# Optimization experiments

Measured on AMD Instinct MI355X. Metric: run time of the kernel, lower is better.

Reference implementation:

```python
import jax, jax.numpy as jnp
import numpy as np

T, B, H = 256, 512, 2048

def setup_inputs() -> dict:
    key = jax.random.key(0)
    ks = jax.random.split(key, 10)
    s = 1.0 / np.sqrt(H)  # torch RNN/Linear init scale (values only need to be sane)
    return {
        "initial_input": jax.random.normal(ks[0], (B, 1), jnp.float32),
        "hidden": jax.random.normal(ks[1], (B, H), jnp.float32),
        "targets": jax.random.normal(ks[2], (T, B, 1), jnp.float32),
        "W_ih": jax.random.normal(ks[3], (H, 1), jnp.float32) * s,
        "b_ih": jax.random.normal(ks[4], (H,), jnp.float32) * s,
        "W_hh": jax.random.normal(ks[5], (H, H), jnp.float32) * s,
        "b_hh": jax.random.normal(ks[6], (H,), jnp.float32) * s,
        "W_out": jax.random.normal(ks[7], (1, H), jnp.float32) * s,
        "b_out": jax.random.normal(ks[8], (1,), jnp.float32) * s,
        "tf_mask": jax.random.randint(ks[9], (T,), 0, 2) > 0,  # per-step teacher-force decision
    }

def reference(initial_input, hidden, targets, W_ih, b_ih, W_hh, b_hh, W_out, b_out, tf_mask):
    def step(carry, xs):
        h, x = carry                      # h: [B,H], x: [B,1]
        tgt, tf = xs                      # tgt: [B,1], tf: scalar bool
        h = jnp.tanh(x @ W_ih.T + b_ih + h @ W_hh.T + b_hh)  # [B,H]
        y = h @ W_out.T + b_out           # [B,1]
        x_next = jnp.where(tf, tgt, y)
        return (h, x_next), y
    (_, _), outputs = jax.lax.scan(step, (hidden, initial_input), (targets, tf_mask))
    return outputs  # [T,B,1]
```

## Files before the change

### kernel.cpp

```cpp
#include <hip/hip_runtime.h>

using half8   = __attribute__((ext_vector_type(8))) _Float16;
using f32x16  = __attribute__((ext_vector_type(16))) float;
using float4v = __attribute__((ext_vector_type(4))) float;

#define T_STEPS 256
#define BATCH   512
#define HID     2048
#define KS      128

__device__ __forceinline__ f32x16 zero16() {
  f32x16 z;
#pragma unroll
  for (int r = 0; r < 16; ++r) z[r] = 0.0f;
  return z;
}

__device__ __forceinline__ half8 load16_sc0(const half8* p) {
  half8 r;
  asm volatile("global_load_dwordx4 %0, %1, off sc0" : "=v"(r) : "v"(p));
  return r;
}
__device__ __forceinline__ float load4_sc0(const float* p) {
  float r;
  asm volatile("global_load_dword %0, %1, off sc0" : "=v"(r) : "v"(p));
  return r;
}

__global__ void pack_whh_k(const float* __restrict__ whh, half8* __restrict__ bp) {
  int id   = blockIdx.x * 256 + threadIdx.x;
  int lane = id & 63;
  int ks   = (id >> 6) & 127;
  int nblk = id >> 13;
  int j = nblk * 32 + (lane & 31);
  int k = ks * 16 + (lane >> 5) * 8;
  const float4v* src = (const float4v*)(whh + (size_t)j * HID + k);
  float4v a = src[0], b = src[1];
  half8 v;
  v[0]=(_Float16)a[0]; v[1]=(_Float16)a[1]; v[2]=(_Float16)a[2]; v[3]=(_Float16)a[3];
  v[4]=(_Float16)b[0]; v[5]=(_Float16)b[1]; v[6]=(_Float16)b[2]; v[7]=(_Float16)b[3];
  bp[id] = v;
}

__global__ void pack_h_k(const float* __restrict__ hsrc, half8* __restrict__ hp) {
  int id   = blockIdx.x * 256 + threadIdx.x;
  int lane = id & 63;
  int ks   = (id >> 6) & 127;
  int bblk = id >> 13;
  int b = bblk * 32 + (lane & 31);
  int k = ks * 16 + (lane >> 5) * 8;
  const float4v* src = (const float4v*)(hsrc + (size_t)b * HID + k);
  float4v a = src[0], c = src[1];
  half8 v;
  v[0]=(_Float16)a[0]; v[1]=(_Float16)a[1]; v[2]=(_Float16)a[2]; v[3]=(_Float16)a[3];
  v[4]=(_Float16)c[0]; v[5]=(_Float16)c[1]; v[6]=(_Float16)c[2]; v[7]=(_Float16)c[3];
  hp[id] = v;
}

__global__ void bias_k(const float* __restrict__ bih, const float* __restrict__ bhh,
                       float* __restrict__ bias) {
  int i = blockIdx.x * 256 + threadIdx.x;
  if (i < HID) bias[i] = bih[i] + bhh[i];
}

__global__ void tf_expand_k(const int* __restrict__ tf, int* __restrict__ tfc,
                            unsigned* __restrict__ bar) {
  __shared__ int fmt;
  if (threadIdx.x == 0) {
    const unsigned* u = (const unsigned*)tf;
    int all01 = 1;
    for (int i = 0; i < 32; ++i) if (u[i] > 1u) all01 = 0;
    if (all01) {
      int odd0 = 1;
      for (int i = 1; i < 32; i += 2) if (u[i] != 0u) odd0 = 0;
      fmt = odd0 ? 2 : 1;
    } else fmt = 0;
  }
  __syncthreads();
  int i = threadIdx.x;
  int v;
  if (fmt == 2)      v = tf[2 * i];
  else if (fmt == 1) v = tf[i];
  else               v = (int)((const unsigned char*)tf)[i];
  tfc[i] = v ? 1 : 0;
  bar[i] = 0u;
}

__global__ __launch_bounds__(512) void rnn_persist(
    const float* __restrict__ x0,   const float* __restrict__ tgt,
    const int*   __restrict__ tfc,  const float* __restrict__ wih,
    const float* __restrict__ wout, const float* __restrict__ bias,
    const float* __restrict__ bout, const half8* __restrict__ wp,
    half8* __restrict__ h0,         half8* __restrict__ h1,
    float* __restrict__ ypg,        float* __restrict__ out,
    unsigned* __restrict__ bar) {
  __shared__ float part[4][64][68];
  __shared__ float hs[64][68];
  __shared__ float xs[64];
  __shared__ float ypart[8][64];
  __shared__ float wih_s[64], wout_s[64], bias_s[64];
  __shared__ int   tfs[T_STEPS];
  __shared__ int   mn_s[2];

  const int tid = threadIdx.x;
  const int w = tid >> 6;
  const int l = tid & 63;
  const int hi = l >> 5;
  const int c = l & 31;

  if (tid == 0) {
    unsigned xcc = __builtin_amdgcn_s_getreg((31 << 11) | (0 << 6) | 20) & 15u;
    unsigned x = xcc & 7u;
    unsigned r = __hip_atomic_fetch_add(&bar[x * 32 + 16], 1u, __ATOMIC_RELAXED,
                                        __HIP_MEMORY_SCOPE_AGENT);
    mn_s[0] = (int)x;
    mn_s[1] = (int)(r & 31u);
  }
  __syncthreads();
  const int m = mn_s[0];
  const int n = mn_s[1];
  const float bo = bout[0];

  if (tid < 64) {
    int j = n * 64 + tid;
    wih_s[tid]  = wih[j];
    wout_s[tid] = wout[j];
    bias_s[tid] = bias[j];
  }
  if (tid < T_STEPS) tfs[tid] = tfc[tid];

  half8 wb0[16], wb1[16];
  {
    const half8* b0p = wp + ((size_t)(2 * n + 0) * KS + w * 16) * 64 + l;
    const half8* b1p = wp + ((size_t)(2 * n + 1) * KS + w * 16) * 64 + l;
#pragma unroll
    for (int i = 0; i < 16; ++i) { wb0[i] = b0p[i * 64]; wb1[i] = b1p[i * 64]; }
  }
  __syncthreads();

  for (int t = 0; t < T_STEPS; ++t) {
    const half8* hr = (t & 1) ? h1 : h0;
    half8*       hw = (t & 1) ? h0 : h1;

    if (tid < 64) {
      float x;
      if (t == 0) {
        x = x0[m * 64 + tid];
      } else {
        const float* yp = ypg + ((size_t)((t - 1) & 1) * 8 + m) * 32 * 64 + tid;
        float a[32];
#pragma unroll
        for (int i = 0; i < 32; ++i) a[i] = load4_sc0(yp + i * 64);
        asm volatile("s_waitcnt vmcnt(0)" ::: "memory");
        __builtin_amdgcn_sched_barrier(0);
        float s = 0.0f;
#pragma unroll
        for (int i = 0; i < 32; ++i) s += a[i];
        float ysum = s + bo;
        if (n == 0) out[(size_t)(t - 1) * BATCH + m * 64 + tid] = ysum;
        x = tfs[t - 1] ? tgt[(size_t)(t - 1) * BATCH + m * 64 + tid] : ysum;
      }
      xs[tid] = x;
    }

    f32x16 acc00 = zero16(), acc01 = zero16(), acc10 = zero16(), acc11 = zero16();
    {
      const half8* a0p = hr + ((size_t)(2 * m + 0) * KS + w * 16) * 64 + l;
      const half8* a1p = hr + ((size_t)(2 * m + 1) * KS + w * 16) * 64 + l;
#pragma unroll
      for (int kk = 0; kk < 4; ++kk) {
        half8 a0[4], a1[4];
#pragma unroll
        for (int i = 0; i < 4; ++i) {
          a0[i] = load16_sc0(a0p + (kk * 4 + i) * 64);
          a1[i] = load16_sc0(a1p + (kk * 4 + i) * 64);
        }
        asm volatile("s_waitcnt vmcnt(0)" ::: "memory");
        __builtin_amdgcn_sched_barrier(0);
#pragma unroll
        for (int i = 0; i < 4; ++i) {
          acc00 = __builtin_amdgcn_mfma_f32_32x32x16_f16(a0[i], wb0[kk * 4 + i], acc00, 0, 0, 0);
          acc01 = __builtin_amdgcn_mfma_f32_32x32x16_f16(a0[i], wb1[kk * 4 + i], acc01, 0, 0, 0);
          acc10 = __builtin_amdgcn_mfma_f32_32x32x16_f16(a1[i], wb0[kk * 4 + i], acc10, 0, 0, 0);
          acc11 = __builtin_amdgcn_mfma_f32_32x32x16_f16(a1[i], wb1[kk * 4 + i], acc11, 0, 0, 0);
        }
      }
    }

    if (w < 4) {
#pragma unroll
      for (int r = 0; r < 16; ++r) {
        int row0 = (r & 3) + 8 * (r >> 2) + 4 * hi;
        part[w][row0     ][c     ] = acc00[r];
        part[w][row0     ][c + 32] = acc01[r];
        part[w][row0 + 32][c     ] = acc10[r];
        part[w][row0 + 32][c + 32] = acc11[r];
      }
    }
    __syncthreads();
    if (w >= 4) {
      int ww = w - 4;
#pragma unroll
      for (int r = 0; r < 16; ++r) {
        int row0 = (r & 3) + 8 * (r >> 2) + 4 * hi;
        part[ww][row0     ][c     ] += acc00[r];
        part[ww][row0     ][c + 32] += acc01[r];
        part[ww][row0 + 32][c     ] += acc10[r];
        part[ww][row0 + 32][c + 32] += acc11[r];
      }
    }
    __syncthreads();

    {
      int mb = w & 1, nb = (w >> 1) & 1, rh = w >> 2;
#pragma unroll
      for (int r = 0; r < 8; ++r) {
        int rr = rh * 8 + r;
        int row = mb * 32 + (rr & 3) + 8 * (rr >> 2) + 4 * hi;
        int col = nb * 32 + c;
        float s = part[0][row][col] + part[1][row][col]
                + part[2][row][col] + part[3][row][col];
        s += bias_s[col] + xs[row] * wih_s[col];
        hs[row][col] = tanhf(s);
      }
    }
    __syncthreads();

    {
      int row = tid & 63;
      int g   = tid >> 6;
      float hv[8];
      float4v v0 = *(const float4v*)&hs[row][g * 8];
      float4v v1 = *(const float4v*)&hs[row][g * 8 + 4];
      hv[0]=v0[0]; hv[1]=v0[1]; hv[2]=v0[2]; hv[3]=v0[3];
      hv[4]=v1[0]; hv[5]=v1[1]; hv[6]=v1[2]; hv[7]=v1[3];

      float yp = 0.0f;
#pragma unroll
      for (int e = 0; e < 8; ++e) yp += hv[e] * wout_s[g * 8 + e];
      ypart[g][row] = yp;

      half8 f;
#pragma unroll
      for (int e = 0; e < 8; ++e) f[e] = (_Float16)hv[e];
      int bblk = 2 * m + (row >> 5);
      int ksg  = n * 4 + (g >> 1);
      int lane = (g & 1) * 32 + (row & 31);
      hw[((size_t)bblk * KS + ksg) * 64 + lane] = f;
    }
    __syncthreads();

    if (w == 0) {
      float y = ypart[0][tid] + ypart[1][tid] + ypart[2][tid] + ypart[3][tid]
              + ypart[4][tid] + ypart[5][tid] + ypart[6][tid] + ypart[7][tid];
      ypg[(((size_t)(t & 1) * 8 + m) * 32 + n) * 64 + tid] = y;
      asm volatile("s_waitcnt vmcnt(0)" ::: "memory");
    }

    if (tid == 0) {
      __hip_atomic_fetch_add(&bar[m * 32], 1u, __ATOMIC_RELAXED,
                             __HIP_MEMORY_SCOPE_AGENT);
      unsigned tgt_cnt = 32u * (unsigned)(t + 1);
      while (__hip_atomic_load(&bar[m * 32], __ATOMIC_RELAXED,
                               __HIP_MEMORY_SCOPE_AGENT) < tgt_cnt)
        __builtin_amdgcn_s_sleep(1);
    }
    __syncthreads();
  }

  if (n == 0 && tid < 64) {
    const float* yp = ypg + ((size_t)((T_STEPS - 1) & 1) * 8 + m) * 32 * 64 + tid;
    float a[32];
#pragma unroll
    for (int i = 0; i < 32; ++i) a[i] = load4_sc0(yp + i * 64);
    asm volatile("s_waitcnt vmcnt(0)" ::: "memory");
    __builtin_amdgcn_sched_barrier(0);
    float s = 0.0f;
#pragma unroll
    for (int i = 0; i < 32; ++i) s += a[i];
    out[(size_t)(T_STEPS - 1) * BATCH + m * 64 + tid] = s + bo;
  }
}

extern "C" void kernel_launch(void* const* d_in, const int* in_sizes, int n_in,
                              void* d_out, int out_size, void* d_ws, size_t ws_size,
                              hipStream_t stream) {
  (void)in_sizes; (void)n_in; (void)out_size; (void)ws_size;
  const float* x0   = (const float*)d_in[0];
  const float* hid  = (const float*)d_in[1];
  const float* tgt  = (const float*)d_in[2];
  const float* wih  = (const float*)d_in[3];
  const float* bih  = (const float*)d_in[4];
  const float* whh  = (const float*)d_in[5];
  const float* bhh  = (const float*)d_in[6];
  const float* wout = (const float*)d_in[7];
  const float* bout = (const float*)d_in[8];
  const int*   tf   = (const int*)d_in[9];
  float* out = (float*)d_out;

  char* ws = (char*)d_ws;
  half8*    wp   = (half8*)ws;
  half8*    h0   = (half8*)(ws + (8u  << 20));
  half8*    h1   = (half8*)(ws + (10u << 20));
  float*    bias = (float*)(ws + (12u << 20));
  int*      tfc  = (int*)  (ws + (12u << 20) + 8192);
  unsigned* bar  = (unsigned*)(ws + (12u << 20) + 16384);
  float*    ypg  = (float*)(ws + (12u << 20) + 32768);

  pack_whh_k <<<2048, 256, 0, stream>>>(whh, wp);
  pack_h_k   <<<512,  256, 0, stream>>>(hid, h0);
  bias_k     <<<8,    256, 0, stream>>>(bih, bhh, bias);
  tf_expand_k<<<1,    256, 0, stream>>>(tf, tfc, bar);

  rnn_persist<<<256, 512, 0, stream>>>(x0, tgt, tfc, wih, wout, bias, bout,
                                       wp, h0, h1, ypg, out, bar);
}
```

Baseline: 2.128 ms.

## Swizzle LDS reduction layout, vectorize partial stores, overlap y gather with MFMA

Replaces the padded row-major LDS partial-sum and hidden-state buffers with an XOR-swizzled column-major float4 layout, so accumulator stores, the cross-wave reduction and the tanh stage use 16-byte LDS accesses. The step's feedback gather of y partials from global memory now runs after the MFMA loop in wave 0, overlapping with other waves' LDS stores instead of delaying the start of the matmul. The MFMA section is also wrapped in s_setprio raises. Together these aim to cut LDS instruction count, bank conflicts and per-step serial latency in the persistent loop, at the cost of more complex indexing.

```diff
diff --git a/kernel.cpp b/kernel.cpp
--- a/kernel.cpp
+++ b/kernel.cpp
@@ -21,7 +21,7 @@
   asm volatile("global_load_dwordx4 %0, %1, off sc0" : "=v"(r) : "v"(p));
   return r;
 }
-__device__ __forceinline__ float load4_sc0(const float* p) {
+__device__ __forceinline__ float loadf_sc0(const float* p) {
   float r;
   asm volatile("global_load_dword %0, %1, off sc0" : "=v"(r) : "v"(p));
   return r;
@@ -86,6 +86,31 @@
   bar[i] = 0u;
 }
 
+#define PART_IDX(W_, COL_, RG_) (((W_) * 64 + (COL_)) * 16 + ((RG_) ^ ((COL_) & 15)))
+
+#define ST_ACC(ACC, AM, AN, SLAB) do {                                     \
+  int col_ = (AN) * 32 + c;                                                \
+  _Pragma("unroll")                                                        \
+  for (int g_ = 0; g_ < 4; ++g_) {                                         \
+    int rg_ = (AM) * 8 + 2 * g_ + hi;                                      \
+    float4v v_;                                                            \
+    v_[0] = (ACC)[4*g_];   v_[1] = (ACC)[4*g_+1];                          \
+    v_[2] = (ACC)[4*g_+2]; v_[3] = (ACC)[4*g_+3];                          \
+    part4[PART_IDX(SLAB, col_, rg_)] = v_;                                 \
+  } } while (0)
+
+#define ADD_ACC(ACC, AM, AN, SLAB) do {                                    \
+  int col_ = (AN) * 32 + c;                                                \
+  _Pragma("unroll")                                                        \
+  for (int g_ = 0; g_ < 4; ++g_) {                                         \
+    int rg_ = (AM) * 8 + 2 * g_ + hi;                                      \
+    int idx_ = PART_IDX(SLAB, col_, rg_);                                  \
+    float4v v_ = part4[idx_];                                              \
+    v_[0] += (ACC)[4*g_];   v_[1] += (ACC)[4*g_+1];                        \
+    v_[2] += (ACC)[4*g_+2]; v_[3] += (ACC)[4*g_+3];                        \
+    part4[idx_] = v_;                                                      \
+  } } while (0)
+
 __global__ __launch_bounds__(512) void rnn_persist(
     const float* __restrict__ x0,   const float* __restrict__ tgt,
     const int*   __restrict__ tfc,  const float* __restrict__ wih,
@@ -94,8 +119,8 @@
     half8* __restrict__ h0,         half8* __restrict__ h1,
     float* __restrict__ ypg,        float* __restrict__ out,
     unsigned* __restrict__ bar) {
-  __shared__ float part[4][64][68];
-  __shared__ float hs[64][68];
+  __shared__ float4v part4[4 * 64 * 16];
+  __shared__ float4v hs4[64 * 16];
   __shared__ float xs[64];
   __shared__ float ypart[8][64];
   __shared__ float wih_s[64], wout_s[64], bias_s[64];
@@ -142,27 +167,6 @@
     const half8* hr = (t & 1) ? h1 : h0;
     half8*       hw = (t & 1) ? h0 : h1;
 
-    if (tid < 64) {
-      float x;
-      if (t == 0) {
-        x = x0[m * 64 + tid];
-      } else {
-        const float* yp = ypg + ((size_t)((t - 1) & 1) * 8 + m) * 32 * 64 + tid;
-        float a[32];
-#pragma unroll
-        for (int i = 0; i < 32; ++i) a[i] = load4_sc0(yp + i * 64);
-        asm volatile("s_waitcnt vmcnt(0)" ::: "memory");
-        __builtin_amdgcn_sched_barrier(0);
-        float s = 0.0f;
-#pragma unroll
-        for (int i = 0; i < 32; ++i) s += a[i];
-        float ysum = s + bo;
-        if (n == 0) out[(size_t)(t - 1) * BATCH + m * 64 + tid] = ysum;
-        x = tfs[t - 1] ? tgt[(size_t)(t - 1) * BATCH + m * 64 + tid] : ysum;
-      }
-      xs[tid] = x;
-    }
-
     f32x16 acc00 = zero16(), acc01 = zero16(), acc10 = zero16(), acc11 = zero16();
     {
       const half8* a0p = hr + ((size_t)(2 * m + 0) * KS + w * 16) * 64 + l;
@@ -177,6 +181,7 @@
         }
         asm volatile("s_waitcnt vmcnt(0)" ::: "memory");
         __builtin_amdgcn_sched_barrier(0);
+        __builtin_amdgcn_s_setprio(1);
 #pragma unroll
         for (int i = 0; i < 4; ++i) {
           acc00 = __builtin_amdgcn_mfma_f32_32x32x16_f16(a0[i], wb0[kk * 4 + i], acc00, 0, 0, 0);
@@ -184,76 +189,101 @@
           acc10 = __builtin_amdgcn_mfma_f32_32x32x16_f16(a1[i], wb0[kk * 4 + i], acc10, 0, 0, 0);
           acc11 = __builtin_amdgcn_mfma_f32_32x32x16_f16(a1[i], wb1[kk * 4 + i], acc11, 0, 0, 0);
         }
+        __builtin_amdgcn_s_setprio(0);
       }
     }
 
     if (w < 4) {
-#pragma unroll
-      for (int r = 0; r < 16; ++r) {
-        int row0 = (r & 3) + 8 * (r >> 2) + 4 * hi;
-        part[w][row0     ][c     ] = acc00[r];
-        part[w][row0     ][c + 32] = acc01[r];
-        part[w][row0 + 32][c     ] = acc10[r];
-        part[w][row0 + 32][c + 32] = acc11[r];
+      ST_ACC(acc00, 0, 0, w); ST_ACC(acc01, 0, 1, w);
+      ST_ACC(acc10, 1, 0, w); ST_ACC(acc11, 1, 1, w);
+    }
+
+    if (w == 0) {
+      float x;
+      if (t == 0) {
+        x = x0[m * 64 + l];
+      } else {
+        const float* yp = ypg + ((size_t)((t - 1) & 1) * 8 + m) * 2048 + l;
+        float a[32];
+#pragma unroll
+        for (int i = 0; i < 32; ++i) a[i] = loadf_sc0(yp + i * 64);
+        asm volatile("s_waitcnt vmcnt(0)" ::: "memory");
+        __builtin_amdgcn_sched_barrier(0);
+        float s = 0.0f;
+#pragma unroll
+        for (int i = 0; i < 32; ++i) s += a[i];
+        float ysum = s + bo;
+        if (n == 0) out[(size_t)(t - 1) * BATCH + m * 64 + l] = ysum;
+        x = tfs[t - 1] ? tgt[(size_t)(t - 1) * BATCH + m * 64 + l] : ysum;
       }
-    }
-    __syncthreads();
+      xs[l] = x;
+    }
+    __syncthreads();
+
     if (w >= 4) {
-      int ww = w - 4;
-#pragma unroll
-      for (int r = 0; r < 16; ++r) {
-        int row0 = (r & 3) + 8 * (r >> 2) + 4 * hi;
-        part[ww][row0     ][c     ] += acc00[r];
-        part[ww][row0     ][c + 32] += acc01[r];
-        part[ww][row0 + 32][c     ] += acc10[r];
-        part[ww][row0 + 32][c + 32] += acc11[r];
-      }
+      int s4 = w - 4;
+      ADD_ACC(acc00, 0, 0, s4); ADD_ACC(acc01, 0, 1, s4);
+      ADD_ACC(acc10, 1, 0, s4); ADD_ACC(acc11, 1, 1, s4);
     }
     __syncthreads();
 
     {
       int mb = w & 1, nb = (w >> 1) & 1, rh = w >> 2;
-#pragma unroll
-      for (int r = 0; r < 8; ++r) {
-        int rr = rh * 8 + r;
-        int row = mb * 32 + (rr & 3) + 8 * (rr >> 2) + 4 * hi;
-        int col = nb * 32 + c;
-        float s = part[0][row][col] + part[1][row][col]
-                + part[2][row][col] + part[3][row][col];
-        s += bias_s[col] + xs[row] * wih_s[col];
-        hs[row][col] = tanhf(s);
+      int col = nb * 32 + c;
+      int cx  = col & 15;
+      int rg0 = mb * 8 + 4 * rh + hi;
+      int rg1 = rg0 + 2;
+      float4v s0 = part4[PART_IDX(0, col, rg0)];
+      s0 += part4[PART_IDX(1, col, rg0)];
+      s0 += part4[PART_IDX(2, col, rg0)];
+      s0 += part4[PART_IDX(3, col, rg0)];
+      float4v s1 = part4[PART_IDX(0, col, rg1)];
+      s1 += part4[PART_IDX(1, col, rg1)];
+      s1 += part4[PART_IDX(2, col, rg1)];
+      s1 += part4[PART_IDX(3, col, rg1)];
+      float bcol = bias_s[col], wcol = wih_s[col];
+      int rb0 = mb * 32 + 16 * rh + 4 * hi;
+      int rb1 = rb0 + 8;
+      float4v h0v, h1v;
+#pragma unroll
+      for (int e = 0; e < 4; ++e) {
+        h0v[e] = tanhf(s0[e] + bcol + xs[rb0 + e] * wcol);
+        h1v[e] = tanhf(s1[e] + bcol + xs[rb1 + e] * wcol);
       }
+      hs4[col * 16 + (rg0 ^ cx)] = h0v;
+      hs4[col * 16 + (rg1 ^ cx)] = h1v;
     }
     __syncthreads();
 
     {
-      int row = tid & 63;
-      int g   = tid >> 6;
+      int row = l;
+      int rg = row >> 2, re = row & 3;
+      const float* hsf = (const float*)hs4;
       float hv[8];
-      float4v v0 = *(const float4v*)&hs[row][g * 8];
-      float4v v1 = *(const float4v*)&hs[row][g * 8 + 4];
-      hv[0]=v0[0]; hv[1]=v0[1]; hv[2]=v0[2]; hv[3]=v0[3];
-      hv[4]=v1[0]; hv[5]=v1[1]; hv[6]=v1[2]; hv[7]=v1[3];
-
+#pragma unroll
+      for (int i = 0; i < 8; ++i) {
+        int col = w * 8 + i;
+        hv[i] = hsf[col * 64 + ((rg ^ (col & 15)) << 2) + re];
+      }
       float yp = 0.0f;
 #pragma unroll
-      for (int e = 0; e < 8; ++e) yp += hv[e] * wout_s[g * 8 + e];
-      ypart[g][row] = yp;
+      for (int e = 0; e < 8; ++e) yp += hv[e] * wout_s[w * 8 + e];
+      ypart[w][row] = yp;
 
       half8 f;
 #pragma unroll
       for (int e = 0; e < 8; ++e) f[e] = (_Float16)hv[e];
       int bblk = 2 * m + (row >> 5);
-      int ksg  = n * 4 + (g >> 1);
-      int lane = (g & 1) * 32 + (row & 31);
+      int ksg  = n * 4 + (w >> 1);
+      int lane = (w & 1) * 32 + (row & 31);
       hw[((size_t)bblk * KS + ksg) * 64 + lane] = f;
     }
     __syncthreads();
 
     if (w == 0) {
-      float y = ypart[0][tid] + ypart[1][tid] + ypart[2][tid] + ypart[3][tid]
-              + ypart[4][tid] + ypart[5][tid] + ypart[6][tid] + ypart[7][tid];
-      ypg[(((size_t)(t & 1) * 8 + m) * 32 + n) * 64 + tid] = y;
+      float y = ypart[0][l] + ypart[1][l] + ypart[2][l] + ypart[3][l]
+              + ypart[4][l] + ypart[5][l] + ypart[6][l] + ypart[7][l];
+      ypg[(((size_t)(t & 1) * 8 + m) * 32 + n) * 64 + l] = y;
       asm volatile("s_waitcnt vmcnt(0)" ::: "memory");
     }
 
@@ -269,10 +299,10 @@
   }
 
   if (n == 0 && tid < 64) {
-    const float* yp = ypg + ((size_t)((T_STEPS - 1) & 1) * 8 + m) * 32 * 64 + tid;
+    const float* yp = ypg + ((size_t)((T_STEPS - 1) & 1) * 8 + m) * 2048 + tid;
     float a[32];
 #pragma unroll
-    for (int i = 0; i < 32; ++i) a[i] = load4_sc0(yp + i * 64);
+    for (int i = 0; i < 32; ++i) a[i] = loadf_sc0(yp + i * 64);
     asm volatile("s_waitcnt vmcnt(0)" ::: "memory");
     __builtin_amdgcn_sched_barrier(0);
     float s = 0.0f;
```

Measured after the change: 2.762 ms. 29.8% more time.
